# Performance work log

Hardware: AMD Instinct MI355X
Metric: run time of the kernel (lower is better)

## Reference

```python
import jax, jax.numpy as jnp
import numpy as np
from math import ceil

W, H, L = 1280, 720, 16
NBW = int(ceil(W / L))   # 80
NBH = int(ceil(H / L))   # 45
NUM_BLOCK = NBW * NBH    # 3600
N_POINTS = 32768


def setup_inputs() -> dict:
    key = jax.random.key(0)
    k1, k2 = jax.random.split(key)
    # points uniform over the screen, radii in ~[1, 31] px
    pos2d = jax.random.uniform(k1, (N_POINTS, 2), dtype=jnp.float32) * jnp.array([W, H], dtype=jnp.float32)
    radius = jax.random.uniform(k2, (N_POINTS,), dtype=jnp.float32) * 30.0 + 1.0
    return {"pos2d": pos2d, "radius": radius}


def reference(pos2d, radius):
    # create_tiles: per-point AABB clamped to screen, truncated to int32
    xmin = jnp.clip(pos2d[:, 0] - radius, 0, W).astype(jnp.int32)  # [N]
    ymin = jnp.clip(pos2d[:, 1] - radius, 0, H).astype(jnp.int32)
    xmax = jnp.clip(pos2d[:, 0] + radius, 0, W).astype(jnp.int32)
    ymax = jnp.clip(pos2d[:, 1] + radius, 0, H).astype(jnp.int32)

    # per-tile bounds for all tiles (get_tl / get_br, vectorized)
    ti = jnp.arange(NUM_BLOCK, dtype=jnp.int32)
    xi = ti // NBH
    yi = ti - xi * NBH
    left = xi * L                                   # [T]
    top = yi * L
    right = jnp.minimum((xi + 1) * L, W)
    bottom = jnp.minimum((yi + 1) * L, H)

    # get_inmask for every tile at once -> [T, N] mask
    otl_x = jnp.maximum(xmin[None, :], left[:, None])
    otl_y = jnp.maximum(ymin[None, :], top[:, None])
    obr_x = jnp.minimum(xmax[None, :], right[:, None])
    obr_y = jnp.minimum(ymax[None, :], bottom[:, None])
    in_mask = (obr_x > otl_x) & (obr_y > otl_y)
    return in_mask
```

## Files before the change

kernel.cpp:

```cpp
#include <hip/hip_runtime.h>
#include <hip/hip_bf16.h>

#define SCREEN_W 1280
#define SCREEN_H 720
#define TILE_L   16
#define NBW      80
#define NBH      45
#define NUM_TILE 3600
#define N_POINTS 32768

typedef int v4i __attribute__((ext_vector_type(4)));

__global__ void aabb_kernel(const float* __restrict__ pos2d,
                            const float* __restrict__ radius,
                            unsigned int* __restrict__ pk) {
    int t = blockIdx.x * blockDim.x + threadIdx.x;
    int n = t * 4;
    if (n >= N_POINTS) return;

    const float4* p4 = (const float4*)(pos2d + 2 * n);
    float4 p01 = p4[0];
    float4 p23 = p4[1];
    float4 r   = *(const float4*)(radius + n);

    float xs[4] = {p01.x, p01.z, p23.x, p23.z};
    float ys[4] = {p01.y, p01.w, p23.y, p23.w};
    float rs[4] = {r.x, r.y, r.z, r.w};

    uint4 outp;
    unsigned int* op = &outp.x;
#pragma unroll
    for (int j = 0; j < 4; ++j) {
        float x = xs[j], y = ys[j], rr = rs[j];
        int xmin = (int)fminf(fmaxf(x - rr, 0.0f), (float)SCREEN_W);
        int ymin = (int)fminf(fmaxf(y - rr, 0.0f), (float)SCREEN_H);
        int xmax = (int)fminf(fmaxf(x + rr, 0.0f), (float)SCREEN_W);
        int ymax = (int)fminf(fmaxf(y + rr, 0.0f), (float)SCREEN_H);
        unsigned int ximin = (unsigned int)(xmin >> 4);
        unsigned int ximax = (unsigned int)((xmax + 15) >> 4);
        unsigned int yimin = (unsigned int)(ymin >> 4);
        unsigned int yimax = (unsigned int)((ymax + 15) >> 4);
        op[j] = ximin | (ximax << 8) | (yimin << 16) | (yimax << 24);
    }
    *(uint4*)(pk + n) = outp;
}

__global__ void __launch_bounds__(256)
mask_kernel(const uint4* __restrict__ pk, int* __restrict__ out) {
    int tile = blockIdx.y;
    int t = blockIdx.x * blockDim.x + threadIdx.x;
    int n = t * 4;

    unsigned int xi = (unsigned int)(tile / NBH);
    unsigned int yi = (unsigned int)(tile - (int)xi * NBH);

    uint4 p = pk[t];
    const unsigned int* pp = &p.x;

    v4i res;
#pragma unroll
    for (int j = 0; j < 4; ++j) {
        unsigned int w = pp[j];
        unsigned int ximin =  w        & 0xFFu;
        unsigned int ximax = (w >> 8)  & 0xFFu;
        unsigned int yimin = (w >> 16) & 0xFFu;
        unsigned int yimax =  w >> 24;
        res[j] = (xi >= ximin && xi < ximax && yi >= yimin && yi < yimax) ? 1 : 0;
    }

    *(v4i*)(out + (size_t)tile * N_POINTS + n) = res;
}

extern "C" void kernel_launch(void* const* d_in, const int* in_sizes, int n_in,
                              void* d_out, int out_size, void* d_ws, size_t ws_size,
                              hipStream_t stream) {
    const float* pos2d  = (const float*)d_in[0];
    const float* radius = (const float*)d_in[1];
    int* out = (int*)d_out;
    unsigned int* pk = (unsigned int*)d_ws;

    aabb_kernel<<<dim3(8192 / 256), dim3(256), 0, stream>>>(pos2d, radius, pk);

    mask_kernel<<<dim3(32, NUM_TILE), dim3(256), 0, stream>>>((const uint4*)pk, out);
}
```

Baseline: 446.5 us.

## Fuse AABB computation into a persistent grid-stride mask kernel

```diff
diff --git a/kernel.cpp b/kernel.cpp
--- a/kernel.cpp
+++ b/kernel.cpp
@@ -11,24 +11,23 @@
 
 typedef int v4i __attribute__((ext_vector_type(4)));
 
-__global__ void aabb_kernel(const float* __restrict__ pos2d,
-                            const float* __restrict__ radius,
-                            unsigned int* __restrict__ pk) {
-    int t = blockIdx.x * blockDim.x + threadIdx.x;
-    int n = t * 4;
-    if (n >= N_POINTS) return;
+__global__ void __launch_bounds__(256)
+fused_mask_kernel(const float* __restrict__ pos2d,
+                  const float* __restrict__ radius,
+                  int* __restrict__ out) {
+    const int lin = blockIdx.x * 256 + (int)threadIdx.x;
+    const int t   = lin & 8191;
+    const int n   = t * 4;
 
-    const float4* p4 = (const float4*)(pos2d + 2 * n);
-    float4 p01 = p4[0];
-    float4 p23 = p4[1];
-    float4 r   = *(const float4*)(radius + n);
+    const float4 p01 = *(const float4*)(pos2d + 2 * n);
+    const float4 p23 = *(const float4*)(pos2d + 2 * n + 4);
+    const float4 r4  = *(const float4*)(radius + n);
 
     float xs[4] = {p01.x, p01.z, p23.x, p23.z};
     float ys[4] = {p01.y, p01.w, p23.y, p23.w};
-    float rs[4] = {r.x, r.y, r.z, r.w};
+    float rs[4] = {r4.x, r4.y, r4.z, r4.w};
 
-    uint4 outp;
-    unsigned int* op = &outp.x;
+    unsigned int xlo[4], xhi[4], ylo[4], yhi[4];
 #pragma unroll
     for (int j = 0; j < 4; ++j) {
         float x = xs[j], y = ys[j], rr = rs[j];
@@ -36,39 +35,30 @@
         int ymin = (int)fminf(fmaxf(y - rr, 0.0f), (float)SCREEN_H);
         int xmax = (int)fminf(fmaxf(x + rr, 0.0f), (float)SCREEN_W);
         int ymax = (int)fminf(fmaxf(y + rr, 0.0f), (float)SCREEN_H);
-        unsigned int ximin = (unsigned int)(xmin >> 4);
-        unsigned int ximax = (unsigned int)((xmax + 15) >> 4);
-        unsigned int yimin = (unsigned int)(ymin >> 4);
-        unsigned int yimax = (unsigned int)((ymax + 15) >> 4);
-        op[j] = ximin | (ximax << 8) | (yimin << 16) | (yimax << 24);
-    }
-    *(uint4*)(pk + n) = outp;
-}
-
-__global__ void __launch_bounds__(256)
-mask_kernel(const uint4* __restrict__ pk, int* __restrict__ out) {
-    int tile = blockIdx.y;
-    int t = blockIdx.x * blockDim.x + threadIdx.x;
-    int n = t * 4;
-
-    unsigned int xi = (unsigned int)(tile / NBH);
-    unsigned int yi = (unsigned int)(tile - (int)xi * NBH);
-
-    uint4 p = pk[t];
-    const unsigned int* pp = &p.x;
-
-    v4i res;
-#pragma unroll
-    for (int j = 0; j < 4; ++j) {
-        unsigned int w = pp[j];
-        unsigned int ximin =  w        & 0xFFu;
-        unsigned int ximax = (w >> 8)  & 0xFFu;
-        unsigned int yimin = (w >> 16) & 0xFFu;
-        unsigned int yimax =  w >> 24;
-        res[j] = (xi >= ximin && xi < ximax && yi >= yimin && yi < yimax) ? 1 : 0;
+        xlo[j] = (unsigned int)(xmin >> 4);
+        xhi[j] = (unsigned int)((xmax + 15) >> 4);
+        ylo[j] = (unsigned int)(ymin >> 4);
+        yhi[j] = (unsigned int)((ymax + 15) >> 4);
     }
 
-    *(v4i*)(out + (size_t)tile * N_POINTS + n) = res;
+    const int TOTAL  = NUM_TILE * (N_POINTS / 4);
+    const int STRIDE = 2048 * 256;
+
+#pragma unroll 4
+    for (int g = lin; g < TOTAL; g += STRIDE) {
+        unsigned int tile = (unsigned int)g >> 13;
+        unsigned int xi = tile / (unsigned int)NBH;
+        unsigned int yi = tile - xi * (unsigned int)NBH;
+
+        v4i res;
+#pragma unroll
+        for (int j = 0; j < 4; ++j) {
+            res[j] = (xi >= xlo[j] && xi < xhi[j] &&
+                      yi >= ylo[j] && yi < yhi[j]) ? 1 : 0;
+        }
+
+        *(v4i*)(out + (size_t)g * 4) = res;
+    }
 }
 
 extern "C" void kernel_launch(void* const* d_in, const int* in_sizes, int n_in,
@@ -77,9 +67,6 @@
     const float* pos2d  = (const float*)d_in[0];
     const float* radius = (const float*)d_in[1];
     int* out = (int*)d_out;
-    unsigned int* pk = (unsigned int*)d_ws;
 
-    aabb_kernel<<<dim3(8192 / 256), dim3(256), 0, stream>>>(pos2d, radius, pk);
-
-    mask_kernel<<<dim3(32, NUM_TILE), dim3(256), 0, stream>>>((const uint4*)pk, out);
+    fused_mask_kernel<<<dim3(2048), dim3(256), 0, stream>>>(pos2d, radius, out);
 }
```

Result: slower. 481.5 us (+7.8%).
